# Performance work log

Measured on AMD Instinct MI355X. Metric: run time of the kernel, lower is better.

Reference implementation:

```python
import jax, jax.numpy as jnp
import numpy as np

B = 16384
ARCHI = [784, 128, 128, 10]
T_STEPS = 60


def setup_inputs() -> dict:
    key = jax.random.key(0)
    ks = jax.random.split(key, 5)
    x = jax.random.normal(ks[0], (B, ARCHI[0]), dtype=jnp.float32)
    y = jax.random.randint(ks[1], (B,), 0, ARCHI[-1], dtype=jnp.int64)
    # Linear weights, torch convention: out = x @ W.T + b, scaled to avoid tanh saturation
    W0 = jax.random.normal(ks[2], (ARCHI[1], ARCHI[0]), dtype=jnp.float32) / np.float32(np.sqrt(ARCHI[0]))
    W1 = jax.random.normal(ks[3], (ARCHI[2], ARCHI[1]), dtype=jnp.float32) / np.float32(np.sqrt(ARCHI[1]))
    W2 = jax.random.normal(ks[4], (ARCHI[3], ARCHI[2]), dtype=jnp.float32) / np.float32(np.sqrt(ARCHI[2]))
    b0 = jnp.zeros((ARCHI[1],), jnp.float32)
    b1 = jnp.zeros((ARCHI[2],), jnp.float32)
    b2 = jnp.zeros((ARCHI[3],), jnp.float32)
    n1 = jnp.zeros((B, ARCHI[1]), jnp.float32)
    n2 = jnp.zeros((B, ARCHI[2]), jnp.float32)
    n3 = jnp.zeros((B, ARCHI[3]), jnp.float32)
    return {"x": x, "y": y, "n1": n1, "n2": n2, "n3": n3,
            "W0": W0, "b0": b0, "W1": W1, "b1": b1, "W2": W2, "b2": b2,
            "T": T_STEPS}


def reference(x, y, n1, n2, n3, W0, b0, W1, b1, W2, b2, T):
    # EqProp relaxation with beta=0 (default forward call). Phi is bilinear in
    # adjacent layers, so torch.autograd.grad(Phi, neurons) has the closed form:
    #   g_j = W_{j-1} h_{j-1} + b_{j-1} + W_j^T h_{j+1}   (last layer drops 2nd term)
    # All neurons are updated synchronously from the previous state, then tanh
    # (MSE criterion branch applies activation to the last layer as well).
    def step(ns, _):
        h1, h2, h3 = ns
        g1 = x @ W0.T + b0 + h2 @ W1   # [B,128]
        g2 = h1 @ W1.T + b1 + h3 @ W2  # [B,128]
        g3 = h2 @ W2.T + b2            # [B,10]
        return (jnp.tanh(g1), jnp.tanh(g2), jnp.tanh(g3)), None

    (h1, h2, h3), _ = jax.lax.scan(step, (n1, n2, n3), None, length=T)
    return (h1, h2, h3)
```

## Files before the change

kernel.cpp:

```cpp
#include <hip/hip_runtime.h>


#define NB 16384
#define D0 784
#define D1 128
#define D3 10
#define TSTEPS 60
#define NT 512
#define ROWS 64
#define NBLK (NB / ROWS)
#define H2O ((size_t)NB * D1)
#define H3O ((size_t)2 * NB * D1)
#define XS_LD 68

__device__ __forceinline__ float ftanh(float x)
{
    float e = __expf(2.0f * x);
    float r = __builtin_amdgcn_rcpf(e + 1.0f);
    return fmaf(-2.0f, r, 1.0f);
}

union F4 { float4 v; float f[4]; };

__global__ __launch_bounds__(NT, 1)
void k_fused(const float* __restrict__ x,
             const float* __restrict__ n1, const float* __restrict__ n2,
             const float* __restrict__ n3,
             const float* __restrict__ W0, const float* __restrict__ b0,
             const float* __restrict__ W1, const float* __restrict__ b1,
             const float* __restrict__ W2, const float* __restrict__ b2,
             float* __restrict__ out)
{
    __shared__ float W1L[D1 * D1];
    __shared__ float h1L[ROWS * D1];
    __shared__ float h2L[ROWS * D1];
    float* xs = W1L;

    const int tid = threadIdx.x;
    const int jg = tid & 31, rg = tid >> 5;
    const int j0 = jg * 4, r0 = rg * 4;
    const int jg3 = (jg < D3) ? jg : 0;
    const size_t row0 = (size_t)blockIdx.x * ROWS;

    float c1r[4][4];
    #pragma unroll
    for (int i = 0; i < 4; ++i)
        #pragma unroll
        for (int l = 0; l < 4; ++l) c1r[i][l] = 0.f;

    for (int ch = 0; ch < 13; ++ch) {
        const int kb = ch * 64;
        const int klen = (ch < 12) ? 64 : 16;
        const int nv4 = klen >> 2;
        for (int q = tid; q < ROWS * nv4; q += NT) {
            int r = q / nv4, c4 = q - r * nv4;
            *(float4*)&xs[r * XS_LD + 4 * c4] =
                *(const float4*)(x + (row0 + r) * D0 + kb + 4 * c4);
        }
        __syncthreads();
        for (int k = 0; k < klen; k += 4) {
            F4 xr[4];
            #pragma unroll
            for (int i = 0; i < 4; ++i)
                xr[i].v = *(const float4*)&xs[(r0 + i) * XS_LD + k];
            #pragma unroll
            for (int l = 0; l < 4; ++l) {
                F4 w; w.v = *(const float4*)(W0 + (size_t)(j0 + l) * D0 + kb + k);
                #pragma unroll
                for (int kk = 0; kk < 4; ++kk)
                    #pragma unroll
                    for (int i = 0; i < 4; ++i)
                        c1r[i][l] = fmaf(xr[i].f[kk], w.f[kk], c1r[i][l]);
            }
        }
        __syncthreads();
    }
    float b1r[4];
    #pragma unroll
    for (int l = 0; l < 4; ++l) {
        float bb = b0[j0 + l];
        #pragma unroll
        for (int i = 0; i < 4; ++i) c1r[i][l] += bb;
        b1r[l] = b1[j0 + l];
    }
    const float b2r = (jg < D3) ? b2[jg] : 0.f;

    for (int q = tid; q < 4096; q += NT) {
        int r = q >> 5, c4 = q & 31;
        int d = (r << 5) | (c4 ^ (r >> 2));
        ((float4*)W1L)[d] = ((const float4*)W1)[q];
    }
    for (int q = tid; q < ROWS * 32; q += NT) {
        int r = q >> 5, c4 = q & 31;
        *(float4*)&h1L[r * D1 + 4 * c4] = *(const float4*)(n1 + (row0 + r) * D1 + 4 * c4);
        *(float4*)&h2L[r * D1 + 4 * c4] = *(const float4*)(n2 + (row0 + r) * D1 + 4 * c4);
    }
    float h3r[4];
    #pragma unroll
    for (int i = 0; i < 4; ++i)
        h3r[i] = (jg < D3) ? n3[(row0 + r0 + i) * D3 + jg] : 0.f;
    __syncthreads();

    for (int t = 0; t < TSTEPS; ++t) {
        float a1[4][4], a2[4][4], a3[4];
        #pragma unroll
        for (int i = 0; i < 4; ++i) {
            #pragma unroll
            for (int l = 0; l < 4; ++l) { a1[i][l] = c1r[i][l]; a2[i][l] = b1r[l]; }
            a3[i] = b2r;
        }

        for (int k = 0; k < D1; k += 4) {
            F4 p2[4], p1[4];
            #pragma unroll
            for (int i = 0; i < 4; ++i) {
                p2[i].v = *(const float4*)&h2L[(r0 + i) * D1 + k];
                p1[i].v = *(const float4*)&h1L[(r0 + i) * D1 + k];
            }
            F4 w2r; w2r.v = *(const float4*)(W2 + (size_t)jg3 * D1 + k);
            const int co = ((jg ^ (k >> 2)) << 2);
            F4 wb[4];
            #pragma unroll
            for (int l = 0; l < 4; ++l)
                wb[l].v = *(const float4*)&W1L[(j0 + l) * D1 + co];
            #pragma unroll
            for (int kk = 0; kk < 4; ++kk) {
                F4 wa;
                wa.v = *(const float4*)&W1L[(k + kk) * D1 + co];
                #pragma unroll
                for (int i = 0; i < 4; ++i) {
                    #pragma unroll
                    for (int l = 0; l < 4; ++l) {
                        a1[i][l] = fmaf(p2[i].f[kk], wa.f[l],     a1[i][l]);
                        a2[i][l] = fmaf(p1[i].f[kk], wb[l].f[kk], a2[i][l]);
                    }
                    a3[i] = fmaf(p2[i].f[kk], w2r.f[kk], a3[i]);
                }
            }
        }
        #pragma unroll
        for (int kk = 0; kk < D3; ++kk) {
            F4 wc; wc.v = *(const float4*)(W2 + (size_t)kk * D1 + j0);
            #pragma unroll
            for (int i = 0; i < 4; ++i) {
                float h3v = __shfl(h3r[i], kk, 32);
                #pragma unroll
                for (int l = 0; l < 4; ++l)
                    a2[i][l] = fmaf(h3v, wc.f[l], a2[i][l]);
            }
        }
        __syncthreads();
        #pragma unroll
        for (int i = 0; i < 4; ++i) {
            *(float4*)&h1L[(r0 + i) * D1 + j0] =
                make_float4(ftanh(a1[i][0]), ftanh(a1[i][1]), ftanh(a1[i][2]), ftanh(a1[i][3]));
            *(float4*)&h2L[(r0 + i) * D1 + j0] =
                make_float4(ftanh(a2[i][0]), ftanh(a2[i][1]), ftanh(a2[i][2]), ftanh(a2[i][3]));
            h3r[i] = ftanh(a3[i]);
        }
        __syncthreads();
    }

    for (int q = tid; q < ROWS * 32; q += NT) {
        int r = q >> 5, c4 = q & 31;
        *(float4*)(out + (row0 + r) * D1 + 4 * c4)       = *(const float4*)&h1L[r * D1 + 4 * c4];
        *(float4*)(out + H2O + (row0 + r) * D1 + 4 * c4) = *(const float4*)&h2L[r * D1 + 4 * c4];
    }
    if (jg < D3) {
        #pragma unroll
        for (int i = 0; i < 4; ++i)
            out[H3O + (row0 + r0 + i) * D3 + jg] = h3r[i];
    }
}

extern "C" void kernel_launch(void* const* d_in, const int* in_sizes, int n_in,
                              void* d_out, int out_size, void* d_ws, size_t ws_size,
                              hipStream_t stream) {
    const float* x  = (const float*)d_in[0];
    const float* n1 = (const float*)d_in[2];
    const float* n2 = (const float*)d_in[3];
    const float* n3 = (const float*)d_in[4];
    const float* W0 = (const float*)d_in[5];
    const float* b0 = (const float*)d_in[6];
    const float* W1 = (const float*)d_in[7];
    const float* b1 = (const float*)d_in[8];
    const float* W2 = (const float*)d_in[9];
    const float* b2 = (const float*)d_in[10];

    k_fused<<<NBLK, NT, 0, stream>>>(x, n1, n2, n3, W0, b0, W1, b1, W2, b2,
                                     (float*)d_out);

    hipError_t e = hipGetLastError();
    if (e != hipSuccess) {
        static float code[4];
        code[0] = code[1] = code[2] = code[3] = 1000.0f + (float)(int)e;
        hipMemcpyAsync(d_out, code, 4 * sizeof(float), hipMemcpyHostToDevice, stream);
    }
}
```

Before: 1.385 ms.

## Split relaxation step across thread halves with 8-row tiles per thread

Half the threads now compute the layer-1 update (h2·W1 plus h3 output) and the other half the layer-2 update (h1·W1ᵀ plus h3·W2). Each thread now covers 8 rows instead of 4, so every W1 fragment loaded from LDS is reused across more rows, which cuts LDS read traffic per FMA. The constant x·W0ᵀ+b0 term moves from registers into a new LDS buffer. h3 now lives in the global output buffer and is re-read from global memory each step. The larger register tile and the extra LDS array raise per-thread register and shared-memory pressure, and the global h3 reads add latency to every step.

```diff
diff --git a/kernel.cpp b/kernel.cpp
--- a/kernel.cpp
+++ b/kernel.cpp
@@ -8,6 +8,7 @@
 #define TSTEPS 60
 #define NT 512
 #define ROWS 64
+#define R 8
 #define NBLK (NB / ROWS)
 #define H2O ((size_t)NB * D1)
 #define H3O ((size_t)2 * NB * D1)
@@ -34,56 +35,59 @@
     __shared__ float W1L[D1 * D1];
     __shared__ float h1L[ROWS * D1];
     __shared__ float h2L[ROWS * D1];
+    __shared__ float c1L[ROWS * D1];
     float* xs = W1L;
 
     const int tid = threadIdx.x;
-    const int jg = tid & 31, rg = tid >> 5;
-    const int j0 = jg * 4, r0 = rg * 4;
+    const int jg = tid & 31;
+    const int j0 = jg * 4;
     const int jg3 = (jg < D3) ? jg : 0;
     const size_t row0 = (size_t)blockIdx.x * ROWS;
 
-    float c1r[4][4];
-    #pragma unroll
-    for (int i = 0; i < 4; ++i)
+    {
+        const int rgp = tid >> 5;
+        const int rp0 = rgp * 4;
+        float c1r[4][4];
         #pragma unroll
-        for (int l = 0; l < 4; ++l) c1r[i][l] = 0.f;
-
-    for (int ch = 0; ch < 13; ++ch) {
-        const int kb = ch * 64;
-        const int klen = (ch < 12) ? 64 : 16;
-        const int nv4 = klen >> 2;
-        for (int q = tid; q < ROWS * nv4; q += NT) {
-            int r = q / nv4, c4 = q - r * nv4;
-            *(float4*)&xs[r * XS_LD + 4 * c4] =
-                *(const float4*)(x + (row0 + r) * D0 + kb + 4 * c4);
-        }
-        __syncthreads();
-        for (int k = 0; k < klen; k += 4) {
-            F4 xr[4];
-            #pragma unroll
-            for (int i = 0; i < 4; ++i)
-                xr[i].v = *(const float4*)&xs[(r0 + i) * XS_LD + k];
-            #pragma unroll
-            for (int l = 0; l < 4; ++l) {
-                F4 w; w.v = *(const float4*)(W0 + (size_t)(j0 + l) * D0 + kb + k);
-                #pragma unroll
-                for (int kk = 0; kk < 4; ++kk)
-                    #pragma unroll
-                    for (int i = 0; i < 4; ++i)
-                        c1r[i][l] = fmaf(xr[i].f[kk], w.f[kk], c1r[i][l]);
-            }
-        }
-        __syncthreads();
-    }
-    float b1r[4];
-    #pragma unroll
-    for (int l = 0; l < 4; ++l) {
-        float bb = b0[j0 + l];
+        for (int i = 0; i < 4; ++i)
+            #pragma unroll
+            for (int l = 0; l < 4; ++l) c1r[i][l] = 0.f;
+
+        for (int ch = 0; ch < 13; ++ch) {
+            const int kb = ch * 64;
+            const int klen = (ch < 12) ? 64 : 16;
+            const int nv4 = klen >> 2;
+            for (int q = tid; q < ROWS * nv4; q += NT) {
+                int r = q / nv4, c4 = q - r * nv4;
+                *(float4*)&xs[r * XS_LD + 4 * c4] =
+                    *(const float4*)(x + (row0 + r) * D0 + kb + 4 * c4);
+            }
+            __syncthreads();
+            for (int k = 0; k < klen; k += 4) {
+                F4 xr[4];
+                #pragma unroll
+                for (int i = 0; i < 4; ++i)
+                    xr[i].v = *(const float4*)&xs[(rp0 + i) * XS_LD + k];
+                #pragma unroll
+                for (int l = 0; l < 4; ++l) {
+                    F4 w; w.v = *(const float4*)(W0 + (size_t)(j0 + l) * D0 + kb + k);
+                    #pragma unroll
+                    for (int kk = 0; kk < 4; ++kk)
+                        #pragma unroll
+                        for (int i = 0; i < 4; ++i)
+                            c1r[i][l] = fmaf(xr[i].f[kk], w.f[kk], c1r[i][l]);
+                }
+            }
+            __syncthreads();
+        }
         #pragma unroll
-        for (int i = 0; i < 4; ++i) c1r[i][l] += bb;
-        b1r[l] = b1[j0 + l];
-    }
-    const float b2r = (jg < D3) ? b2[jg] : 0.f;
+        for (int i = 0; i < 4; ++i) {
+            F4 cv;
+            #pragma unroll
+            for (int l = 0; l < 4; ++l) cv.f[l] = c1r[i][l] + b0[j0 + l];
+            *(float4*)&c1L[(rp0 + i) * D1 + j0] = cv.v;
+        }
+    }
 
     for (int q = tid; q < 4096; q += NT) {
         int r = q >> 5, c4 = q & 31;
@@ -95,68 +99,100 @@
         *(float4*)&h1L[r * D1 + 4 * c4] = *(const float4*)(n1 + (row0 + r) * D1 + 4 * c4);
         *(float4*)&h2L[r * D1 + 4 * c4] = *(const float4*)(n2 + (row0 + r) * D1 + 4 * c4);
     }
-    float h3r[4];
+    for (int q = tid; q < ROWS * D3; q += NT)
+        out[H3O + (row0 + q / D3) * D3 + (q % D3)] = n3[(row0 + q / D3) * D3 + (q % D3)];
+    __syncthreads();
+
+    const int rga = (tid >> 5) & 7;
+    const int r0 = rga * R;
+    const bool taskA = (tid < 256);
+    float b1r[4];
     #pragma unroll
-    for (int i = 0; i < 4; ++i)
-        h3r[i] = (jg < D3) ? n3[(row0 + r0 + i) * D3 + jg] : 0.f;
-    __syncthreads();
+    for (int l = 0; l < 4; ++l) b1r[l] = b1[j0 + l];
+    const float b2r = (jg < D3) ? b2[jg] : 0.f;
 
     for (int t = 0; t < TSTEPS; ++t) {
-        float a1[4][4], a2[4][4], a3[4];
-        #pragma unroll
-        for (int i = 0; i < 4; ++i) {
-            #pragma unroll
-            for (int l = 0; l < 4; ++l) { a1[i][l] = c1r[i][l]; a2[i][l] = b1r[l]; }
-            a3[i] = b2r;
-        }
-
-        for (int k = 0; k < D1; k += 4) {
-            F4 p2[4], p1[4];
-            #pragma unroll
-            for (int i = 0; i < 4; ++i) {
-                p2[i].v = *(const float4*)&h2L[(r0 + i) * D1 + k];
-                p1[i].v = *(const float4*)&h1L[(r0 + i) * D1 + k];
-            }
-            F4 w2r; w2r.v = *(const float4*)(W2 + (size_t)jg3 * D1 + k);
-            const int co = ((jg ^ (k >> 2)) << 2);
-            F4 wb[4];
-            #pragma unroll
-            for (int l = 0; l < 4; ++l)
-                wb[l].v = *(const float4*)&W1L[(j0 + l) * D1 + co];
-            #pragma unroll
-            for (int kk = 0; kk < 4; ++kk) {
-                F4 wa;
-                wa.v = *(const float4*)&W1L[(k + kk) * D1 + co];
-                #pragma unroll
-                for (int i = 0; i < 4; ++i) {
-                    #pragma unroll
-                    for (int l = 0; l < 4; ++l) {
-                        a1[i][l] = fmaf(p2[i].f[kk], wa.f[l],     a1[i][l]);
-                        a2[i][l] = fmaf(p1[i].f[kk], wb[l].f[kk], a2[i][l]);
+        float acc[R][4];
+        float a3[R];
+        if (taskA) {
+            #pragma unroll
+            for (int i = 0; i < R; ++i) {
+                F4 cv; cv.v = *(const float4*)&c1L[(r0 + i) * D1 + j0];
+                #pragma unroll
+                for (int l = 0; l < 4; ++l) acc[i][l] = cv.f[l];
+                a3[i] = b2r;
+            }
+            for (int c = 0; c < 32; ++c) {
+                const int k = c << 2, co = (jg ^ c) << 2;
+                F4 wa[4], p2[R], w2r;
+                #pragma unroll
+                for (int kk = 0; kk < 4; ++kk)
+                    wa[kk].v = *(const float4*)&W1L[(k + kk) * D1 + co];
+                #pragma unroll
+                for (int i = 0; i < R; ++i)
+                    p2[i].v = *(const float4*)&h2L[(r0 + i) * D1 + k];
+                w2r.v = *(const float4*)(W2 + (size_t)jg3 * D1 + k);
+                #pragma unroll
+                for (int kk = 0; kk < 4; ++kk)
+                    #pragma unroll
+                    for (int i = 0; i < R; ++i) {
+                        #pragma unroll
+                        for (int l = 0; l < 4; ++l)
+                            acc[i][l] = fmaf(p2[i].f[kk], wa[kk].f[l], acc[i][l]);
+                        a3[i] = fmaf(p2[i].f[kk], w2r.f[kk], a3[i]);
                     }
-                    a3[i] = fmaf(p2[i].f[kk], w2r.f[kk], a3[i]);
+            }
+        } else {
+            #pragma unroll
+            for (int i = 0; i < R; ++i)
+                #pragma unroll
+                for (int l = 0; l < 4; ++l) acc[i][l] = b1r[l];
+            for (int c = 0; c < 32; ++c) {
+                const int k = c << 2, co = (jg ^ c) << 2;
+                F4 wb[4], p1[R];
+                #pragma unroll
+                for (int l = 0; l < 4; ++l)
+                    wb[l].v = *(const float4*)&W1L[(j0 + l) * D1 + co];
+                #pragma unroll
+                for (int i = 0; i < R; ++i)
+                    p1[i].v = *(const float4*)&h1L[(r0 + i) * D1 + k];
+                #pragma unroll
+                for (int kk = 0; kk < 4; ++kk)
+                    #pragma unroll
+                    for (int i = 0; i < R; ++i)
+                        #pragma unroll
+                        for (int l = 0; l < 4; ++l)
+                            acc[i][l] = fmaf(p1[i].f[kk], wb[l].f[kk], acc[i][l]);
+            }
+            for (int kk = 0; kk < D3; ++kk) {
+                F4 wc; wc.v = *(const float4*)(W2 + (size_t)kk * D1 + j0);
+                #pragma unroll
+                for (int i = 0; i < R; ++i) {
+                    float h3v = out[H3O + (row0 + r0 + i) * D3 + kk];
+                    #pragma unroll
+                    for (int l = 0; l < 4; ++l)
+                        acc[i][l] = fmaf(h3v, wc.f[l], acc[i][l]);
                 }
             }
         }
-        #pragma unroll
-        for (int kk = 0; kk < D3; ++kk) {
-            F4 wc; wc.v = *(const float4*)(W2 + (size_t)kk * D1 + j0);
-            #pragma unroll
-            for (int i = 0; i < 4; ++i) {
-                float h3v = __shfl(h3r[i], kk, 32);
-                #pragma unroll
-                for (int l = 0; l < 4; ++l)
-                    a2[i][l] = fmaf(h3v, wc.f[l], a2[i][l]);
-            }
-        }
         __syncthreads();
-        #pragma unroll
-        for (int i = 0; i < 4; ++i) {
-            *(float4*)&h1L[(r0 + i) * D1 + j0] =
-                make_float4(ftanh(a1[i][0]), ftanh(a1[i][1]), ftanh(a1[i][2]), ftanh(a1[i][3]));
-            *(float4*)&h2L[(r0 + i) * D1 + j0] =
-                make_float4(ftanh(a2[i][0]), ftanh(a2[i][1]), ftanh(a2[i][2]), ftanh(a2[i][3]));
-            h3r[i] = ftanh(a3[i]);
+        if (taskA) {
+            #pragma unroll
+            for (int i = 0; i < R; ++i)
+                *(float4*)&h1L[(r0 + i) * D1 + j0] =
+                    make_float4(ftanh(acc[i][0]), ftanh(acc[i][1]),
+                                ftanh(acc[i][2]), ftanh(acc[i][3]));
+            if (jg < D3) {
+                #pragma unroll
+                for (int i = 0; i < R; ++i)
+                    out[H3O + (row0 + r0 + i) * D3 + jg] = ftanh(a3[i]);
+            }
+        } else {
+            #pragma unroll
+            for (int i = 0; i < R; ++i)
+                *(float4*)&h2L[(r0 + i) * D1 + j0] =
+                    make_float4(ftanh(acc[i][0]), ftanh(acc[i][1]),
+                                ftanh(acc[i][2]), ftanh(acc[i][3]));
         }
         __syncthreads();
     }
@@ -165,11 +201,6 @@
         int r = q >> 5, c4 = q & 31;
         *(float4*)(out + (row0 + r) * D1 + 4 * c4)       = *(const float4*)&h1L[r * D1 + 4 * c4];
         *(float4*)(out + H2O + (row0 + r) * D1 + 4 * c4) = *(const float4*)&h2L[r * D1 + 4 * c4];
-    }
-    if (jg < D3) {
-        #pragma unroll
-        for (int i = 0; i < 4; ++i)
-            out[H3O + (row0 + r0 + i) * D3 + jg] = h3r[i];
     }
 }
 
```

New measurement: 1.301 ms. 6.1% less time.
